# Performance work log

Measured on AMD Instinct MI355X. Metric: run time of the kernel, lower is better.

Reference implementation:

```python
import jax, jax.numpy as jnp
import numpy as np

N = 64        # n_nodes per graph
H = 128       # hidden channels (128x0e + 128x1o)
NB = 8        # radial bessel basis size
L = 2         # num_interactions
R_MAX = 5.0
AVG_NEIGH = 63.0
DIM = 3       # output vector dim
B = 64        # batch (vmapped)
T = 32        # time-embedding dim
S = 5         # num_species


def _edges(n):
    # fully-connected graph, no self loops (static shapes, jit-friendly)
    s, r = np.meshgrid(np.arange(n), np.arange(n), indexing='ij')
    m = s != r
    return jnp.asarray(s[m]), jnp.asarray(r[m])


def setup_inputs() -> dict:
    key = jax.random.key(0)
    ks = jax.random.split(key, 12)
    sc = 0.05
    return {
        'positions': jax.random.normal(ks[0], (B, N, 3), jnp.float32),
        'node_features': jax.random.randint(ks[1], (B, N), 0, S).astype(jnp.int64),
        'global_features': jax.random.normal(ks[2], (B, T), jnp.float32),
        'emb': jax.random.normal(ks[3], (S, H), jnp.float32) * sc,
        'Wt': jax.random.normal(ks[4], (T, H), jnp.float32) * sc,
        'Wr1': jax.random.normal(ks[5], (L, NB, H), jnp.float32) * sc,
        'Wr2': jax.random.normal(ks[6], (L, H, H), jnp.float32) * sc,
        'Wupd': jax.random.normal(ks[7], (L, H, H), jnp.float32) * sc,
        'Wmix': jax.random.normal(ks[8], (L, H, H), jnp.float32) * sc,
        'Wg1': jax.random.normal(ks[9], (H, H), jnp.float32) * sc,
        'Wg2': jax.random.normal(ks[10], (H, H), jnp.float32) * sc,
        'final_scaling': jnp.ones((), jnp.float32),
    }


def _call_single(pos, z, t, emb, Wt, Wr1, Wr2, Wupd, Wmix, Wg1, Wg2, final_scaling):
    snd, rcv = _edges(N)
    ev = pos[rcv] - pos[snd]                               # [E,3] edge vectors (gather)
    r = jnp.sqrt(jnp.sum(ev * ev, axis=-1) + 1e-12)        # [E]
    u = ev / r[:, None]                                    # unit directions
    # Bessel radial basis with cosine cutoff (r_max acts as soft radius graph)
    n = jnp.arange(1, NB + 1, dtype=pos.dtype)
    rb = jnp.sin(n * jnp.pi * r[:, None] / R_MAX) / r[:, None]   # [E,NB]
    fc = 0.5 * (jnp.cos(jnp.pi * r / R_MAX) + 1.0) * (r < R_MAX)
    rb = rb * fc[:, None]
    # node embedding from species + time embedding
    h = emb[z] + t @ Wt                                    # [N,H] scalar features
    v = jnp.zeros((N, H, DIM), pos.dtype)                  # vector (1o) features
    for l in range(L):
        w = jax.nn.silu(rb @ Wr1[l]) @ Wr2[l]              # [E,H] radial weights
        m0 = w * h[snd]                                    # [E,H] scalar messages
        m1 = m0[:, :, None] * u[:, None, :]                # [E,H,3] vector messages
        a0 = jax.ops.segment_sum(m0, rcv, num_segments=N) / AVG_NEIGH
        a1 = jax.ops.segment_sum(m1, rcv, num_segments=N) / AVG_NEIGH
        h = h + a0 @ Wupd[l]
        v = v + jnp.einsum('ngd,gh->nhd', a1, Wmix[l])
    # equivariant readout: scalar gate per channel contracts vector channels
    g = jax.nn.silu(h @ Wg1) @ Wg2                         # [N,H]
    out = jnp.einsum('nhd,nh->nd', v, g)                   # [N,3]
    return out * final_scaling


def reference(positions, node_features, global_features, emb, Wt, Wr1, Wr2, Wupd, Wmix, Wg1, Wg2, final_scaling):
    f = lambda p, z, t: _call_single(p, z, t, emb, Wt, Wr1, Wr2, Wupd, Wmix, Wg1, Wg2, final_scaling)
    return jax.vmap(f)(positions, node_features, global_features)
```

## Files before the change

kernel.cpp:

```cpp
#include <hip/hip_runtime.h>
#include <math.h>

#define NN 64
#define HH 128
#define NBB 8
#define TT 32
#define BB 64
#define NROW (BB * NN)
#define PLANE ((size_t)NROW * HH)
#define WR1OFF (8 * 16384)

typedef __attribute__((ext_vector_type(8))) short short8;
typedef __attribute__((ext_vector_type(4))) float f32x4;
typedef __attribute__((ext_vector_type(2))) float f32x2;
typedef __attribute__((ext_vector_type(2))) unsigned int u32x2;

__device__ __forceinline__ float silu_f(float x) {
  return x * __builtin_amdgcn_rcpf(1.0f + __expf(-x));
}

__device__ __forceinline__ unsigned short bf1(float x) {
  __bf16 h = (__bf16)x;
  return *(unsigned short*)&h;
}
__device__ __forceinline__ unsigned bf2(float lo, float hi) {
  return (unsigned)bf1(lo) | ((unsigned)bf1(hi) << 16);
}

__device__ __forceinline__ void gemm8(
    const unsigned short (*sA)[136], const unsigned short* __restrict__ Bp,
    int w, int nlo, int quad, f32x4 C[2]) {
  const short8 z8 = {0, 0, 0, 0, 0, 0, 0, 0};
  short8 afr[4];
#pragma unroll
  for (int kt = 0; kt < 4; ++kt)
    afr[kt] = (nlo < 8) ? *(const short8*)&sA[nlo][kt * 32 + quad * 8] : z8;
#pragma unroll
  for (int nt = 0; nt < 2; ++nt)
#pragma unroll
    for (int kt = 0; kt < 4; ++kt) {
      short8 bfr = *(const short8*)&Bp[((kt * 128 + w * 32 + nt * 16 + nlo) * 4 + quad) * 8];
      C[nt] = __builtin_amdgcn_mfma_f32_16x16x32_bf16(afr[kt], bfr, C[nt], 0, 0, 0);
    }
}

__global__ __launch_bounds__(256) void k_init(
    const float* __restrict__ emb, const int* __restrict__ z,
    const float* __restrict__ gf, const float* __restrict__ Wt,
    const float* __restrict__ Wr1, const float* __restrict__ Wr2,
    const float* __restrict__ Wupd, const float* __restrict__ Wmix,
    const float* __restrict__ Wg1, const float* __restrict__ Wg2,
    float* __restrict__ h, unsigned short* __restrict__ Wpack) {
  __shared__ float tvec[HH];
  __shared__ int sz[NN];
  int b4 = blockIdx.x, tid = threadIdx.x;
  {
    int p2 = b4 * 256 + tid;
    int p = p2 * 2;
    int m = p >> 14;
    int j = p & 7;
    int q = (p >> 3) & 3;
    int n = (p >> 5) & 127;
    int kt = (p >> 12) & 3;
    int k = kt * 32 + q * 8 + j;
    const float* src;
    int base;
    if (m < 2) { src = Wr2; base = m * 16384; }
    else if (m < 4) { src = Wupd; base = (m - 2) * 16384; }
    else if (m < 6) { src = Wmix; base = (m - 4) * 16384; }
    else if (m == 6) { src = Wg1; base = 0; }
    else { src = Wg2; base = 0; }
    float v0 = src[base + k * 128 + n];
    float v1 = src[base + (k + 1) * 128 + n];
    *(unsigned*)&Wpack[p] = bf2(v0, v1);
  }
  if (tid < 32) {
    int e = b4 * 32 + tid;
    int l = e >> 12, p = e & 4095;
    int n = p >> 5, q = (p >> 3) & 3, j = p & 7;
    float val = (q == 0) ? Wr1[l * NBB * HH + j * HH + n] : 0.f;
    Wpack[WR1OFF + l * 4096 + p] = bf1(val);
  }
  if (b4 < 64) {
    int b = b4;
    if (tid < NN) sz[tid] = z[b * NN + tid];
    if (tid < HH) {
      float acc = 0.f;
#pragma unroll
      for (int k = 0; k < TT; ++k) acc += gf[b * TT + k] * Wt[k * HH + tid];
      tvec[tid] = acc;
    }
    __syncthreads();
    for (int i = tid; i < NN * HH; i += 256) {
      int n = i >> 7, c = i & 127;
      h[(size_t)b * NN * HH + i] = emb[sz[n] * HH + c] + tvec[c];
    }
  }
}

__global__ __launch_bounds__(256) void k_layer(
    const float* __restrict__ pos,
    const float* __restrict__ hA,
    const unsigned short* __restrict__ a0in,
    unsigned short* __restrict__ apout,
    const unsigned short* __restrict__ Wpack,
    int l) {
  __shared__ __align__(16) unsigned short sh_S[NN][136];
  __shared__ __align__(16) unsigned short sh_M0T[4][32][72];
  __shared__ __align__(16) unsigned short sh_rbh[2][NN][8];
  __shared__ __align__(16) unsigned short sh_ub[2][4][NN];

  int blk = blockIdx.x;
  int b = blk >> 4, rp4 = blk & 15;
  int r0 = rp4 * 4;
  int tid = threadIdx.x;
  int w = tid >> 6, lane = tid & 63;
  int nlo = lane & 15, quad = lane >> 4;

  f32x4 hbv[4][2];
#pragma unroll
  for (int mt = 0; mt < 4; ++mt)
#pragma unroll
    for (int nt = 0; nt < 2; ++nt)
#pragma unroll
      for (int reg = 0; reg < 4; ++reg)
        hbv[mt][nt][reg] =
            hA[((size_t)b * NN + mt * 16 + quad * 4 + reg) * HH + w * 32 + nt * 16 + nlo];

  const unsigned short* Wr1p = Wpack + WR1OFF + l * 4096;
  short8 bw[2];
#pragma unroll
  for (int nt = 0; nt < 2; ++nt)
    bw[nt] = *(const short8*)&Wr1p[((w * 32 + nt * 16 + nlo) * 4 + quad) * 8];
  const unsigned short* Bbase = Wpack + l * 16384;
  short8 bfr[4][2];
#pragma unroll
  for (int kt = 0; kt < 4; ++kt)
#pragma unroll
    for (int nt = 0; nt < 2; ++nt)
      bfr[kt][nt] = *(const short8*)&Bbase[((kt * 128 + w * 32 + nt * 16 + nlo) * 4 + quad) * 8];

  const short8 zero8 = {0, 0, 0, 0, 0, 0, 0, 0};

#pragma unroll
  for (int pp = 0; pp < 2; ++pp) {
    int rb0 = r0 + pp * 2;

    {
      int s = tid & 63;
      int ksel = (tid >> 6) & 1;
      int ri = (tid >> 7) & 1;
      int r = rb0 + ri;
      const float* pb = pos + b * NN * 3;
      float dx = pb[r * 3 + 0] - pb[s * 3 + 0];
      float dy = pb[r * 3 + 1] - pb[s * 3 + 1];
      float dz = pb[r * 3 + 2] - pb[s * 3 + 2];
      float rr = sqrtf(dx * dx + dy * dy + dz * dz + 1e-12f);
      float inv = __builtin_amdgcn_rcpf(rr);
      const float invAvg = 1.0f / 63.0f;
      if (ksel == 0) {
        float ia = inv * invAvg;
        sh_ub[ri][1][s] = bf1(dx * ia);
        sh_ub[ri][2][s] = bf1(dy * ia);
        sh_ub[ri][3][s] = bf1(dz * ia);
      } else {
        sh_ub[ri][0][s] = bf1(invAvg);
      }
      const float PI_OVER_5 = 0.628318530717958647692f;
      float fc = (s != r && rr < 5.0f) ? 0.5f * (__cosf(PI_OVER_5 * rr) + 1.0f) : 0.0f;
      float base = PI_OVER_5 * rr;
      float sc = inv * fc;
      int k0 = ksel * 4;
      float v0 = __sinf((float)(k0 + 1) * base) * sc;
      float v1 = __sinf((float)(k0 + 2) * base) * sc;
      float v2 = __sinf((float)(k0 + 3) * base) * sc;
      float v3 = __sinf((float)(k0 + 4) * base) * sc;
      *(unsigned*)&sh_rbh[ri][s][k0]     = bf2(v0, v1);
      *(unsigned*)&sh_rbh[ri][s][k0 + 2] = bf2(v2, v3);
    }
    if (pp == 0 && l) {
      for (int i = tid; i < NN * 64; i += 256) {
        int s = i >> 6, c2 = (i & 63) * 2;
        *(unsigned*)&sh_S[s][c2] =
            *(const unsigned*)&a0in[((size_t)b * NN + s) * HH + c2];
      }
    }
    __syncthreads();

    if (pp == 0 && l) {
      const unsigned short* Bu = Wpack + 2 * 16384;
#pragma unroll
      for (int mt = 0; mt < 4; ++mt) {
        short8 afr[4];
#pragma unroll
        for (int kt = 0; kt < 4; ++kt)
          afr[kt] = *(const short8*)&sh_S[mt * 16 + nlo][kt * 32 + quad * 8];
#pragma unroll
        for (int nt = 0; nt < 2; ++nt)
#pragma unroll
          for (int kt = 0; kt < 4; ++kt) {
            short8 bfr2 = *(const short8*)&Bu[((kt * 128 + w * 32 + nt * 16 + nlo) * 4 + quad) * 8];
            hbv[mt][nt] = __builtin_amdgcn_mfma_f32_16x16x32_bf16(afr[kt], bfr2, hbv[mt][nt], 0, 0, 0);
          }
      }
      __syncthreads();
    }

    short8 au[2][2];
#pragma unroll
    for (int ri = 0; ri < 2; ++ri)
#pragma unroll
      for (int kt = 0; kt < 2; ++kt)
        au[ri][kt] = (nlo < 4) ? *(const short8*)&sh_ub[ri][nlo][kt * 32 + quad * 8] : zero8;

#pragma unroll
    for (int ri = 0; ri < 2; ++ri) {
#pragma unroll
      for (int mtp = 0; mtp < 2; ++mtp) {
        f32x4 Cs[2][2];
#pragma unroll
        for (int mi = 0; mi < 2; ++mi)
#pragma unroll
          for (int nt = 0; nt < 2; ++nt) Cs[mi][nt] = (f32x4){0.f, 0.f, 0.f, 0.f};
#pragma unroll
        for (int mi = 0; mi < 2; ++mi) {
          int mt = mtp * 2 + mi;
          short8 afr = (quad == 0) ? *(const short8*)&sh_rbh[ri][mt * 16 + nlo][0] : zero8;
#pragma unroll
          for (int nt = 0; nt < 2; ++nt)
            Cs[mi][nt] = __builtin_amdgcn_mfma_f32_16x16x32_bf16(afr, bw[nt], Cs[mi][nt], 0, 0, 0);
        }
#pragma unroll
        for (int mi = 0; mi < 2; ++mi)
#pragma unroll
          for (int nt = 0; nt < 2; ++nt)
#pragma unroll
            for (int reg = 0; reg < 4; ++reg) {
              int s = (mtp * 2 + mi) * 16 + quad * 4 + reg;
              int c = w * 32 + nt * 16 + nlo;
              sh_S[s][c] = bf1(silu_f(Cs[mi][nt][reg]));
            }
      }
      __syncthreads();

#pragma unroll
      for (int mt = 0; mt < 4; ++mt) {
        short8 afr[4];
        int s_a = mt * 16 + nlo;
#pragma unroll
        for (int kt = 0; kt < 4; ++kt)
          afr[kt] = *(const short8*)&sh_S[s_a][kt * 32 + quad * 8];
#pragma unroll
        for (int nt = 0; nt < 2; ++nt) {
          f32x4 C = {0.f, 0.f, 0.f, 0.f};
#pragma unroll
          for (int kt = 0; kt < 4; ++kt)
            C = __builtin_amdgcn_mfma_f32_16x16x32_bf16(afr[kt], bfr[kt][nt], C, 0, 0, 0);
          f32x4 m0 = C * hbv[mt][nt];
          u32x2 pk;
          pk.x = bf2(m0[0], m0[1]);
          pk.y = bf2(m0[2], m0[3]);
          *(u32x2*)&sh_M0T[w][nt * 16 + nlo][mt * 16 + quad * 4] = pk;
        }
      }
      {
        f32x4 Cu[2] = {{0, 0, 0, 0}, {0, 0, 0, 0}};
#pragma unroll
        for (int nt = 0; nt < 2; ++nt)
#pragma unroll
          for (int kt = 0; kt < 2; ++kt) {
            short8 bm = *(const short8*)&sh_M0T[w][nt * 16 + nlo][kt * 32 + quad * 8];
            Cu[nt] = __builtin_amdgcn_mfma_f32_16x16x32_bf16(au[ri][kt], bm, Cu[nt], 0, 0, 0);
          }
        if (quad == 0) {
#pragma unroll
          for (int nt = 0; nt < 2; ++nt) {
            size_t base = (size_t)(b * NN + rb0 + ri) * HH + w * 32 + nt * 16 + nlo;
#pragma unroll
            for (int reg = 0; reg < 4; ++reg)
              apout[(l * 4 + reg) * PLANE + base] = bf1(Cu[nt][reg]);
          }
        }
      }
      if (!(pp == 1 && ri == 1)) __syncthreads();
    }
  }
}

__global__ __launch_bounds__(256) void k_update_ro(
    const unsigned short* __restrict__ apbf, const float* __restrict__ hA,
    const unsigned short* __restrict__ Wpack,
    const float* __restrict__ fs, float* __restrict__ out) {
  __shared__ __align__(16) unsigned short sh_a[8][8][136];
  __shared__ __align__(16) unsigned short sh_h[8][136];
  __shared__ float red[4][8][3];
  int tid = threadIdx.x, w = tid >> 6, lane = tid & 63;
  int nlo = lane & 15, quad = lane >> 4;
  int row0 = blockIdx.x * 8;
  for (int i = tid; i < 8 * 8 * 64; i += 256) {
    int p = i >> 9, rr = (i >> 6) & 7, c2 = (i & 63) * 2;
    *(unsigned*)&sh_a[p][rr][c2] =
        *(const unsigned*)&apbf[p * PLANE + (size_t)(row0 + rr) * HH + c2];
  }
  f32x4 Ch[2];
#pragma unroll
  for (int nt = 0; nt < 2; ++nt)
#pragma unroll
    for (int reg = 0; reg < 4; ++reg)
      Ch[nt][reg] = (quad < 2)
          ? hA[(size_t)(row0 + quad * 4 + reg) * HH + w * 32 + nt * 16 + nlo] : 0.f;
  __syncthreads();
  gemm8(sh_a[0], Wpack + 2 * 16384, w, nlo, quad, Ch);
  gemm8(sh_a[4], Wpack + 3 * 16384, w, nlo, quad, Ch);
  f32x4 Cx[2] = {{0,0,0,0},{0,0,0,0}};
  f32x4 Cy[2] = {{0,0,0,0},{0,0,0,0}};
  f32x4 Cz[2] = {{0,0,0,0},{0,0,0,0}};
  gemm8(sh_a[1], Wpack + 4 * 16384, w, nlo, quad, Cx);
  gemm8(sh_a[5], Wpack + 5 * 16384, w, nlo, quad, Cx);
  gemm8(sh_a[2], Wpack + 4 * 16384, w, nlo, quad, Cy);
  gemm8(sh_a[6], Wpack + 5 * 16384, w, nlo, quad, Cy);
  gemm8(sh_a[3], Wpack + 4 * 16384, w, nlo, quad, Cz);
  gemm8(sh_a[7], Wpack + 5 * 16384, w, nlo, quad, Cz);
  if (quad < 2) {
#pragma unroll
    for (int nt = 0; nt < 2; ++nt)
#pragma unroll
      for (int reg = 0; reg < 4; ++reg)
        sh_h[quad * 4 + reg][w * 32 + nt * 16 + nlo] = bf1(Ch[nt][reg]);
  }
  __syncthreads();
  unsigned short (*sh_q)[136] = sh_a[0];
  f32x4 Cq[2] = {{0,0,0,0},{0,0,0,0}};
  gemm8(sh_h, Wpack + 6 * 16384, w, nlo, quad, Cq);
  if (quad < 2) {
#pragma unroll
    for (int nt = 0; nt < 2; ++nt)
#pragma unroll
      for (int reg = 0; reg < 4; ++reg)
        sh_q[quad * 4 + reg][w * 32 + nt * 16 + nlo] = bf1(silu_f(Cq[nt][reg]));
  }
  __syncthreads();
  f32x4 Cg[2] = {{0,0,0,0},{0,0,0,0}};
  gemm8(sh_q, Wpack + 7 * 16384, w, nlo, quad, Cg);
  float pr[3][4];
#pragma unroll
  for (int d = 0; d < 3; ++d)
#pragma unroll
    for (int reg = 0; reg < 4; ++reg) pr[d][reg] = 0.f;
#pragma unroll
  for (int nt = 0; nt < 2; ++nt)
#pragma unroll
    for (int reg = 0; reg < 4; ++reg) {
      float gv = Cg[nt][reg];
      pr[0][reg] += gv * Cx[nt][reg];
      pr[1][reg] += gv * Cy[nt][reg];
      pr[2][reg] += gv * Cz[nt][reg];
    }
#pragma unroll
  for (int off = 1; off < 16; off <<= 1)
#pragma unroll
    for (int d = 0; d < 3; ++d)
#pragma unroll
      for (int reg = 0; reg < 4; ++reg)
        pr[d][reg] += __shfl_xor(pr[d][reg], off);
  if (nlo == 0 && quad < 2) {
#pragma unroll
    for (int d = 0; d < 3; ++d)
#pragma unroll
      for (int reg = 0; reg < 4; ++reg)
        red[w][quad * 4 + reg][d] = pr[d][reg];
  }
  __syncthreads();
  if (tid < 24) {
    int row = tid / 3, d = tid % 3;
    float s = red[0][row][d] + red[1][row][d] + red[2][row][d] + red[3][row][d];
    out[(size_t)(row0 + row) * 3 + d] = s * fs[0];
  }
}

extern "C" void kernel_launch(void* const* d_in, const int* in_sizes, int n_in,
                              void* d_out, int out_size, void* d_ws, size_t ws_size,
                              hipStream_t stream) {
  const float* pos  = (const float*)d_in[0];
  const int*   z    = (const int*)d_in[1];
  const float* gf   = (const float*)d_in[2];
  const float* emb  = (const float*)d_in[3];
  const float* Wt   = (const float*)d_in[4];
  const float* Wr1  = (const float*)d_in[5];
  const float* Wr2  = (const float*)d_in[6];
  const float* Wupd = (const float*)d_in[7];
  const float* Wmix = (const float*)d_in[8];
  const float* Wg1  = (const float*)d_in[9];
  const float* Wg2  = (const float*)d_in[10];
  const float* fs   = (const float*)d_in[11];
  float* out = (float*)d_out;

  float* ws = (float*)d_ws;
  float* hA = ws;
  unsigned short* apbf = (unsigned short*)(ws + PLANE);
  unsigned short* Wpack = (unsigned short*)(ws + 5 * PLANE);

  k_init<<<dim3(256), dim3(256), 0, stream>>>(emb, z, gf, Wt, Wr1, Wr2, Wupd,
                                              Wmix, Wg1, Wg2, hA, Wpack);
  k_layer<<<dim3(BB * 16), dim3(256), 0, stream>>>(pos, hA, apbf, apbf, Wpack, 0);
  k_layer<<<dim3(BB * 16), dim3(256), 0, stream>>>(pos, hA, apbf, apbf, Wpack, 1);
  k_update_ro<<<dim3(512), dim3(256), 0, stream>>>(apbf, hA, Wpack, fs, out);
}
```

Baseline: 146.3 us.

## Replace MFMA edge-reduction with register shuffle reduction and double-buffer radial stage

The per-receiver aggregation over senders, previously done by writing bf16 messages to shared memory and running an extra MFMA against a unit-vector matrix, now happens in fp32 registers with cross-lane shuffles. Unit vectors are stored as fp32 in shared memory. The radial SiLU buffer is double-buffered so the second receiver's radial stage can run before the first receiver's main GEMM, which removes a barrier. Launch bounds now request 4 blocks per SM, which may force register spilling given the large register-resident fragments.

```diff
diff --git a/kernel.cpp b/kernel.cpp
--- a/kernel.cpp
+++ b/kernel.cpp
@@ -98,17 +98,16 @@
   }
 }
 
-__global__ __launch_bounds__(256) void k_layer(
+__global__ __launch_bounds__(256, 4) void k_layer(
     const float* __restrict__ pos,
     const float* __restrict__ hA,
     const unsigned short* __restrict__ a0in,
     unsigned short* __restrict__ apout,
     const unsigned short* __restrict__ Wpack,
     int l) {
-  __shared__ __align__(16) unsigned short sh_S[NN][136];
-  __shared__ __align__(16) unsigned short sh_M0T[4][32][72];
+  __shared__ __align__(16) unsigned short sh_S[2][NN][136];
   __shared__ __align__(16) unsigned short sh_rbh[2][NN][8];
-  __shared__ __align__(16) unsigned short sh_ub[2][4][NN];
+  __shared__ __align__(16) float sh_uf[2][NN][4];
 
   int blk = blockIdx.x;
   int b = blk >> 4, rp4 = blk & 15;
@@ -116,6 +115,7 @@
   int tid = threadIdx.x;
   int w = tid >> 6, lane = tid & 63;
   int nlo = lane & 15, quad = lane >> 4;
+  const float invAvg = 1.0f / 63.0f;
 
   f32x4 hbv[4][2];
 #pragma unroll
@@ -141,6 +141,82 @@
       bfr[kt][nt] = *(const short8*)&Bbase[((kt * 128 + w * 32 + nt * 16 + nlo) * 4 + quad) * 8];
 
   const short8 zero8 = {0, 0, 0, 0, 0, 0, 0, 0};
+
+  auto stageB = [&](int ri, int buf) {
+#pragma unroll
+    for (int mtp = 0; mtp < 2; ++mtp) {
+      f32x4 Cs[2][2];
+#pragma unroll
+      for (int mi = 0; mi < 2; ++mi)
+#pragma unroll
+        for (int nt = 0; nt < 2; ++nt) Cs[mi][nt] = (f32x4){0.f, 0.f, 0.f, 0.f};
+#pragma unroll
+      for (int mi = 0; mi < 2; ++mi) {
+        int mt = mtp * 2 + mi;
+        short8 afr = (quad == 0) ? *(const short8*)&sh_rbh[ri][mt * 16 + nlo][0] : zero8;
+#pragma unroll
+        for (int nt = 0; nt < 2; ++nt)
+          Cs[mi][nt] = __builtin_amdgcn_mfma_f32_16x16x32_bf16(afr, bw[nt], Cs[mi][nt], 0, 0, 0);
+      }
+#pragma unroll
+      for (int mi = 0; mi < 2; ++mi)
+#pragma unroll
+        for (int nt = 0; nt < 2; ++nt)
+#pragma unroll
+          for (int reg = 0; reg < 4; ++reg) {
+            int s = (mtp * 2 + mi) * 16 + quad * 4 + reg;
+            int c = w * 32 + nt * 16 + nlo;
+            sh_S[buf][s][c] = bf1(silu_f(Cs[mi][nt][reg]));
+          }
+    }
+  };
+
+  auto mainG = [&](int ri, int buf, int rglob) {
+    float a0[2] = {0.f, 0.f};
+    float a1[2][3] = {{0.f, 0.f, 0.f}, {0.f, 0.f, 0.f}};
+#pragma unroll
+    for (int mt = 0; mt < 4; ++mt) {
+      short8 afr[4];
+      int s_a = mt * 16 + nlo;
+#pragma unroll
+      for (int kt = 0; kt < 4; ++kt)
+        afr[kt] = *(const short8*)&sh_S[buf][s_a][kt * 32 + quad * 8];
+      f32x4 u3[4];
+#pragma unroll
+      for (int reg = 0; reg < 4; ++reg)
+        u3[reg] = *(const f32x4*)&sh_uf[ri][mt * 16 + quad * 4 + reg][0];
+#pragma unroll
+      for (int nt = 0; nt < 2; ++nt) {
+        f32x4 C = {0.f, 0.f, 0.f, 0.f};
+#pragma unroll
+        for (int kt = 0; kt < 4; ++kt)
+          C = __builtin_amdgcn_mfma_f32_16x16x32_bf16(afr[kt], bfr[kt][nt], C, 0, 0, 0);
+#pragma unroll
+        for (int reg = 0; reg < 4; ++reg) {
+          float m0 = C[reg] * hbv[mt][nt][reg];
+          a0[nt] += m0;
+          a1[nt][0] += u3[reg][0] * m0;
+          a1[nt][1] += u3[reg][1] * m0;
+          a1[nt][2] += u3[reg][2] * m0;
+        }
+      }
+    }
+#pragma unroll
+    for (int nt = 0; nt < 2; ++nt) {
+      float v0 = a0[nt], v1 = a1[nt][0], v2 = a1[nt][1], v3 = a1[nt][2];
+      v0 += __shfl_xor(v0, 16); v0 += __shfl_xor(v0, 32);
+      v1 += __shfl_xor(v1, 16); v1 += __shfl_xor(v1, 32);
+      v2 += __shfl_xor(v2, 16); v2 += __shfl_xor(v2, 32);
+      v3 += __shfl_xor(v3, 16); v3 += __shfl_xor(v3, 32);
+      if (quad == 0) {
+        size_t base = (size_t)(b * NN + rglob) * HH + w * 32 + nt * 16 + nlo;
+        apout[(l * 4 + 0) * PLANE + base] = bf1(v0 * invAvg);
+        apout[(l * 4 + 1) * PLANE + base] = bf1(v1);
+        apout[(l * 4 + 2) * PLANE + base] = bf1(v2);
+        apout[(l * 4 + 3) * PLANE + base] = bf1(v3);
+      }
+    }
+  };
 
 #pragma unroll
   for (int pp = 0; pp < 2; ++pp) {
@@ -157,14 +233,11 @@
       float dz = pb[r * 3 + 2] - pb[s * 3 + 2];
       float rr = sqrtf(dx * dx + dy * dy + dz * dz + 1e-12f);
       float inv = __builtin_amdgcn_rcpf(rr);
-      const float invAvg = 1.0f / 63.0f;
       if (ksel == 0) {
         float ia = inv * invAvg;
-        sh_ub[ri][1][s] = bf1(dx * ia);
-        sh_ub[ri][2][s] = bf1(dy * ia);
-        sh_ub[ri][3][s] = bf1(dz * ia);
-      } else {
-        sh_ub[ri][0][s] = bf1(invAvg);
+        sh_uf[ri][s][0] = dx * ia;
+        sh_uf[ri][s][1] = dy * ia;
+        sh_uf[ri][s][2] = dz * ia;
       }
       const float PI_OVER_5 = 0.628318530717958647692f;
       float fc = (s != r && rr < 5.0f) ? 0.5f * (__cosf(PI_OVER_5 * rr) + 1.0f) : 0.0f;
@@ -181,7 +254,7 @@
     if (pp == 0 && l) {
       for (int i = tid; i < NN * 64; i += 256) {
         int s = i >> 6, c2 = (i & 63) * 2;
-        *(unsigned*)&sh_S[s][c2] =
+        *(unsigned*)&sh_S[0][s][c2] =
             *(const unsigned*)&a0in[((size_t)b * NN + s) * HH + c2];
       }
     }
@@ -194,7 +267,7 @@
         short8 afr[4];
 #pragma unroll
         for (int kt = 0; kt < 4; ++kt)
-          afr[kt] = *(const short8*)&sh_S[mt * 16 + nlo][kt * 32 + quad * 8];
+          afr[kt] = *(const short8*)&sh_S[0][mt * 16 + nlo][kt * 32 + quad * 8];
 #pragma unroll
         for (int nt = 0; nt < 2; ++nt)
 #pragma unroll
@@ -206,84 +279,13 @@
       __syncthreads();
     }
 
-    short8 au[2][2];
-#pragma unroll
-    for (int ri = 0; ri < 2; ++ri)
-#pragma unroll
-      for (int kt = 0; kt < 2; ++kt)
-        au[ri][kt] = (nlo < 4) ? *(const short8*)&sh_ub[ri][nlo][kt * 32 + quad * 8] : zero8;
-
-#pragma unroll
-    for (int ri = 0; ri < 2; ++ri) {
-#pragma unroll
-      for (int mtp = 0; mtp < 2; ++mtp) {
-        f32x4 Cs[2][2];
-#pragma unroll
-        for (int mi = 0; mi < 2; ++mi)
-#pragma unroll
-          for (int nt = 0; nt < 2; ++nt) Cs[mi][nt] = (f32x4){0.f, 0.f, 0.f, 0.f};
-#pragma unroll
-        for (int mi = 0; mi < 2; ++mi) {
-          int mt = mtp * 2 + mi;
-          short8 afr = (quad == 0) ? *(const short8*)&sh_rbh[ri][mt * 16 + nlo][0] : zero8;
-#pragma unroll
-          for (int nt = 0; nt < 2; ++nt)
-            Cs[mi][nt] = __builtin_amdgcn_mfma_f32_16x16x32_bf16(afr, bw[nt], Cs[mi][nt], 0, 0, 0);
-        }
-#pragma unroll
-        for (int mi = 0; mi < 2; ++mi)
-#pragma unroll
-          for (int nt = 0; nt < 2; ++nt)
-#pragma unroll
-            for (int reg = 0; reg < 4; ++reg) {
-              int s = (mtp * 2 + mi) * 16 + quad * 4 + reg;
-              int c = w * 32 + nt * 16 + nlo;
-              sh_S[s][c] = bf1(silu_f(Cs[mi][nt][reg]));
-            }
-      }
-      __syncthreads();
-
-#pragma unroll
-      for (int mt = 0; mt < 4; ++mt) {
-        short8 afr[4];
-        int s_a = mt * 16 + nlo;
-#pragma unroll
-        for (int kt = 0; kt < 4; ++kt)
-          afr[kt] = *(const short8*)&sh_S[s_a][kt * 32 + quad * 8];
-#pragma unroll
-        for (int nt = 0; nt < 2; ++nt) {
-          f32x4 C = {0.f, 0.f, 0.f, 0.f};
-#pragma unroll
-          for (int kt = 0; kt < 4; ++kt)
-            C = __builtin_amdgcn_mfma_f32_16x16x32_bf16(afr[kt], bfr[kt][nt], C, 0, 0, 0);
-          f32x4 m0 = C * hbv[mt][nt];
-          u32x2 pk;
-          pk.x = bf2(m0[0], m0[1]);
-          pk.y = bf2(m0[2], m0[3]);
-          *(u32x2*)&sh_M0T[w][nt * 16 + nlo][mt * 16 + quad * 4] = pk;
-        }
-      }
-      {
-        f32x4 Cu[2] = {{0, 0, 0, 0}, {0, 0, 0, 0}};
-#pragma unroll
-        for (int nt = 0; nt < 2; ++nt)
-#pragma unroll
-          for (int kt = 0; kt < 2; ++kt) {
-            short8 bm = *(const short8*)&sh_M0T[w][nt * 16 + nlo][kt * 32 + quad * 8];
-            Cu[nt] = __builtin_amdgcn_mfma_f32_16x16x32_bf16(au[ri][kt], bm, Cu[nt], 0, 0, 0);
-          }
-        if (quad == 0) {
-#pragma unroll
-          for (int nt = 0; nt < 2; ++nt) {
-            size_t base = (size_t)(b * NN + rb0 + ri) * HH + w * 32 + nt * 16 + nlo;
-#pragma unroll
-            for (int reg = 0; reg < 4; ++reg)
-              apout[(l * 4 + reg) * PLANE + base] = bf1(Cu[nt][reg]);
-          }
-        }
-      }
-      if (!(pp == 1 && ri == 1)) __syncthreads();
-    }
+    stageB(0, 0);
+    __syncthreads();
+    stageB(1, 1);
+    mainG(0, 0, rb0 + 0);
+    __syncthreads();
+    mainG(1, 1, rb0 + 1);
+    if (pp == 0) __syncthreads();
   }
 }
 
```

After: 222.6 us. 52.1% more time.

## Swizzle LDS tiles, vectorize update staging loads, spread init embedding work

Applied to the files above, without the earlier changes.

Applies an XOR swizzle to column indices of the shared-memory A-operand tiles (sh_S, sh_a, sh_h, sh_q), so MFMA fragment reads and scalar scatter writes spread across LDS banks. Replaces the 4-byte staging loop in the update/readout kernel with 16-byte vector loads and stores. Spreads the node-embedding initialization across all init blocks, 16 nodes each, instead of only the first 64 blocks. The swizzle has to be applied consistently at every read and write site; a missed site would silently corrupt results.

```diff
diff --git a/kernel.cpp b/kernel.cpp
--- a/kernel.cpp
+++ b/kernel.cpp
@@ -10,7 +10,10 @@
 #define PLANE ((size_t)NROW * HH)
 #define WR1OFF (8 * 16384)
 
+#define SWZ(s, c) ((c) ^ (((s) & 7) << 4))
+
 typedef __attribute__((ext_vector_type(8))) short short8;
+typedef __attribute__((ext_vector_type(8))) unsigned short ushort8;
 typedef __attribute__((ext_vector_type(4))) float f32x4;
 typedef __attribute__((ext_vector_type(2))) float f32x2;
 typedef __attribute__((ext_vector_type(2))) unsigned int u32x2;
@@ -34,7 +37,7 @@
   short8 afr[4];
 #pragma unroll
   for (int kt = 0; kt < 4; ++kt)
-    afr[kt] = (nlo < 8) ? *(const short8*)&sA[nlo][kt * 32 + quad * 8] : z8;
+    afr[kt] = (nlo < 8) ? *(const short8*)&sA[nlo][SWZ(nlo, kt * 32 + quad * 8)] : z8;
 #pragma unroll
   for (int nt = 0; nt < 2; ++nt)
 #pragma unroll
@@ -52,7 +55,7 @@
     const float* __restrict__ Wg1, const float* __restrict__ Wg2,
     float* __restrict__ h, unsigned short* __restrict__ Wpack) {
   __shared__ float tvec[HH];
-  __shared__ int sz[NN];
+  __shared__ int sz[16];
   int b4 = blockIdx.x, tid = threadIdx.x;
   {
     int p2 = b4 * 256 + tid;
@@ -81,9 +84,10 @@
     float val = (q == 0) ? Wr1[l * NBB * HH + j * HH + n] : 0.f;
     Wpack[WR1OFF + l * 4096 + p] = bf1(val);
   }
-  if (b4 < 64) {
-    int b = b4;
-    if (tid < NN) sz[tid] = z[b * NN + tid];
+  {
+    int b = b4 >> 2;
+    int n0 = (b4 & 3) * 16;
+    if (tid < 16) sz[tid] = z[b * NN + n0 + tid];
     if (tid < HH) {
       float acc = 0.f;
 #pragma unroll
@@ -91,9 +95,9 @@
       tvec[tid] = acc;
     }
     __syncthreads();
-    for (int i = tid; i < NN * HH; i += 256) {
+    for (int i = tid; i < 16 * HH; i += 256) {
       int n = i >> 7, c = i & 127;
-      h[(size_t)b * NN * HH + i] = emb[sz[n] * HH + c] + tvec[c];
+      h[(size_t)b * NN * HH + (n0 + n) * HH + c] = emb[sz[n] * HH + c] + tvec[c];
     }
   }
 }
@@ -181,7 +185,7 @@
     if (pp == 0 && l) {
       for (int i = tid; i < NN * 64; i += 256) {
         int s = i >> 6, c2 = (i & 63) * 2;
-        *(unsigned*)&sh_S[s][c2] =
+        *(unsigned*)&sh_S[s][SWZ(s, c2)] =
             *(const unsigned*)&a0in[((size_t)b * NN + s) * HH + c2];
       }
     }
@@ -192,9 +196,10 @@
 #pragma unroll
       for (int mt = 0; mt < 4; ++mt) {
         short8 afr[4];
+        int s_a = mt * 16 + nlo;
 #pragma unroll
         for (int kt = 0; kt < 4; ++kt)
-          afr[kt] = *(const short8*)&sh_S[mt * 16 + nlo][kt * 32 + quad * 8];
+          afr[kt] = *(const short8*)&sh_S[s_a][SWZ(s_a, kt * 32 + quad * 8)];
 #pragma unroll
         for (int nt = 0; nt < 2; ++nt)
 #pragma unroll
@@ -238,7 +243,7 @@
             for (int reg = 0; reg < 4; ++reg) {
               int s = (mtp * 2 + mi) * 16 + quad * 4 + reg;
               int c = w * 32 + nt * 16 + nlo;
-              sh_S[s][c] = bf1(silu_f(Cs[mi][nt][reg]));
+              sh_S[s][SWZ(s, c)] = bf1(silu_f(Cs[mi][nt][reg]));
             }
       }
       __syncthreads();
@@ -249,7 +254,7 @@
         int s_a = mt * 16 + nlo;
 #pragma unroll
         for (int kt = 0; kt < 4; ++kt)
-          afr[kt] = *(const short8*)&sh_S[s_a][kt * 32 + quad * 8];
+          afr[kt] = *(const short8*)&sh_S[s_a][SWZ(s_a, kt * 32 + quad * 8)];
 #pragma unroll
         for (int nt = 0; nt < 2; ++nt) {
           f32x4 C = {0.f, 0.f, 0.f, 0.f};
@@ -297,10 +302,12 @@
   int tid = threadIdx.x, w = tid >> 6, lane = tid & 63;
   int nlo = lane & 15, quad = lane >> 4;
   int row0 = blockIdx.x * 8;
-  for (int i = tid; i < 8 * 8 * 64; i += 256) {
-    int p = i >> 9, rr = (i >> 6) & 7, c2 = (i & 63) * 2;
-    *(unsigned*)&sh_a[p][rr][c2] =
-        *(const unsigned*)&apbf[p * PLANE + (size_t)(row0 + rr) * HH + c2];
+#pragma unroll
+  for (int it = 0; it < 4; ++it) {
+    int i2 = it * 256 + tid;
+    int p = i2 >> 7, rr = (i2 >> 4) & 7, c8 = (i2 & 15) * 8;
+    *(ushort8*)&sh_a[p][rr][SWZ(rr, c8)] =
+        *(const ushort8*)&apbf[p * PLANE + (size_t)(row0 + rr) * HH + c8];
   }
   f32x4 Ch[2];
 #pragma unroll
@@ -325,8 +332,10 @@
 #pragma unroll
     for (int nt = 0; nt < 2; ++nt)
 #pragma unroll
-      for (int reg = 0; reg < 4; ++reg)
-        sh_h[quad * 4 + reg][w * 32 + nt * 16 + nlo] = bf1(Ch[nt][reg]);
+      for (int reg = 0; reg < 4; ++reg) {
+        int row = quad * 4 + reg, c = w * 32 + nt * 16 + nlo;
+        sh_h[row][SWZ(row, c)] = bf1(Ch[nt][reg]);
+      }
   }
   __syncthreads();
   unsigned short (*sh_q)[136] = sh_a[0];
@@ -336,8 +345,10 @@
 #pragma unroll
     for (int nt = 0; nt < 2; ++nt)
 #pragma unroll
-      for (int reg = 0; reg < 4; ++reg)
-        sh_q[quad * 4 + reg][w * 32 + nt * 16 + nlo] = bf1(silu_f(Cq[nt][reg]));
+      for (int reg = 0; reg < 4; ++reg) {
+        int row = quad * 4 + reg, c = w * 32 + nt * 16 + nlo;
+        sh_q[row][SWZ(row, c)] = bf1(silu_f(Cq[nt][reg]));
+      }
   }
   __syncthreads();
   f32x4 Cg[2] = {{0,0,0,0},{0,0,0,0}};
```

After: 151.5 us. +3.6%, slower.

## Fuse second interaction layer with update and readout into one kernel

Applied to the files above, without the earlier changes.

Splits the generic layer kernel into a layer-0 kernel and a fused kernel. The fused kernel runs layer 1 for 8 receiver rows per block, then runs the update and readout stage for those same 8 rows, which that block just wrote. This removes one kernel launch and its inter-kernel barrier. It also halves the redundant per-block recomputation of the layer-1 node update (a0·Wupd over all 64 nodes), since 8 blocks per graph do it instead of 16. In exchange, layer 1 runs on half as many blocks, each doing twice the serial work.

```diff
diff --git a/kernel.cpp b/kernel.cpp
--- a/kernel.cpp
+++ b/kernel.cpp
@@ -12,7 +12,6 @@
 
 typedef __attribute__((ext_vector_type(8))) short short8;
 typedef __attribute__((ext_vector_type(4))) float f32x4;
-typedef __attribute__((ext_vector_type(2))) float f32x2;
 typedef __attribute__((ext_vector_type(2))) unsigned int u32x2;
 
 __device__ __forceinline__ float silu_f(float x) {
@@ -98,13 +97,9 @@
   }
 }
 
-__global__ __launch_bounds__(256) void k_layer(
-    const float* __restrict__ pos,
-    const float* __restrict__ hA,
-    const unsigned short* __restrict__ a0in,
-    unsigned short* __restrict__ apout,
-    const unsigned short* __restrict__ Wpack,
-    int l) {
+__global__ __launch_bounds__(256) void k_layer0(
+    const float* __restrict__ pos, const float* __restrict__ hA,
+    unsigned short* __restrict__ apout, const unsigned short* __restrict__ Wpack) {
   __shared__ __align__(16) unsigned short sh_S[NN][136];
   __shared__ __align__(16) unsigned short sh_M0T[4][32][72];
   __shared__ __align__(16) unsigned short sh_rbh[2][NN][8];
@@ -127,12 +122,12 @@
         hbv[mt][nt][reg] =
             hA[((size_t)b * NN + mt * 16 + quad * 4 + reg) * HH + w * 32 + nt * 16 + nlo];
 
-  const unsigned short* Wr1p = Wpack + WR1OFF + l * 4096;
+  const unsigned short* Wr1p = Wpack + WR1OFF;
   short8 bw[2];
 #pragma unroll
   for (int nt = 0; nt < 2; ++nt)
     bw[nt] = *(const short8*)&Wr1p[((w * 32 + nt * 16 + nlo) * 4 + quad) * 8];
-  const unsigned short* Bbase = Wpack + l * 16384;
+  const unsigned short* Bbase = Wpack;
   short8 bfr[4][2];
 #pragma unroll
   for (int kt = 0; kt < 4; ++kt)
@@ -145,7 +140,6 @@
 #pragma unroll
   for (int pp = 0; pp < 2; ++pp) {
     int rb0 = r0 + pp * 2;
-
     {
       int s = tid & 63;
       int ksel = (tid >> 6) & 1;
@@ -178,33 +172,7 @@
       *(unsigned*)&sh_rbh[ri][s][k0]     = bf2(v0, v1);
       *(unsigned*)&sh_rbh[ri][s][k0 + 2] = bf2(v2, v3);
     }
-    if (pp == 0 && l) {
-      for (int i = tid; i < NN * 64; i += 256) {
-        int s = i >> 6, c2 = (i & 63) * 2;
-        *(unsigned*)&sh_S[s][c2] =
-            *(const unsigned*)&a0in[((size_t)b * NN + s) * HH + c2];
-      }
-    }
     __syncthreads();
-
-    if (pp == 0 && l) {
-      const unsigned short* Bu = Wpack + 2 * 16384;
-#pragma unroll
-      for (int mt = 0; mt < 4; ++mt) {
-        short8 afr[4];
-#pragma unroll
-        for (int kt = 0; kt < 4; ++kt)
-          afr[kt] = *(const short8*)&sh_S[mt * 16 + nlo][kt * 32 + quad * 8];
-#pragma unroll
-        for (int nt = 0; nt < 2; ++nt)
-#pragma unroll
-          for (int kt = 0; kt < 4; ++kt) {
-            short8 bfr2 = *(const short8*)&Bu[((kt * 128 + w * 32 + nt * 16 + nlo) * 4 + quad) * 8];
-            hbv[mt][nt] = __builtin_amdgcn_mfma_f32_16x16x32_bf16(afr[kt], bfr2, hbv[mt][nt], 0, 0, 0);
-          }
-      }
-      __syncthreads();
-    }
 
     short8 au[2][2];
 #pragma unroll
@@ -278,7 +246,7 @@
             size_t base = (size_t)(b * NN + rb0 + ri) * HH + w * 32 + nt * 16 + nlo;
 #pragma unroll
             for (int reg = 0; reg < 4; ++reg)
-              apout[(l * 4 + reg) * PLANE + base] = bf1(Cu[nt][reg]);
+              apout[reg * PLANE + base] = bf1(Cu[nt][reg]);
           }
         }
       }
@@ -287,94 +255,275 @@
   }
 }
 
-__global__ __launch_bounds__(256) void k_update_ro(
-    const unsigned short* __restrict__ apbf, const float* __restrict__ hA,
-    const unsigned short* __restrict__ Wpack,
+__global__ __launch_bounds__(256) void k_fused(
+    const float* __restrict__ pos, const float* __restrict__ hA,
+    unsigned short* __restrict__ apbf, const unsigned short* __restrict__ Wpack,
     const float* __restrict__ fs, float* __restrict__ out) {
-  __shared__ __align__(16) unsigned short sh_a[8][8][136];
-  __shared__ __align__(16) unsigned short sh_h[8][136];
-  __shared__ float red[4][8][3];
-  int tid = threadIdx.x, w = tid >> 6, lane = tid & 63;
+  __shared__ __align__(16) unsigned char smem[38912];
+  unsigned short (*sh_S)[136]      = (unsigned short (*)[136])smem;
+  unsigned short (*sh_M0T)[32][72] = (unsigned short (*)[32][72])(smem + 17408);
+  unsigned short (*sh_rbh)[NN][8]  = (unsigned short (*)[NN][8])(smem + 35840);
+  unsigned short (*sh_ub)[4][NN]   = (unsigned short (*)[4][NN])(smem + 37888);
+
+  int blk = blockIdx.x;
+  int b = blk >> 3, u8 = blk & 7;
+  int tid = threadIdx.x;
+  int w = tid >> 6, lane = tid & 63;
   int nlo = lane & 15, quad = lane >> 4;
-  int row0 = blockIdx.x * 8;
-  for (int i = tid; i < 8 * 8 * 64; i += 256) {
-    int p = i >> 9, rr = (i >> 6) & 7, c2 = (i & 63) * 2;
-    *(unsigned*)&sh_a[p][rr][c2] =
-        *(const unsigned*)&apbf[p * PLANE + (size_t)(row0 + rr) * HH + c2];
-  }
-  f32x4 Ch[2];
+  const short8 zero8 = {0, 0, 0, 0, 0, 0, 0, 0};
+
+  f32x4 hbv[4][2];
+#pragma unroll
+  for (int mt = 0; mt < 4; ++mt)
+#pragma unroll
+    for (int nt = 0; nt < 2; ++nt)
+#pragma unroll
+      for (int reg = 0; reg < 4; ++reg)
+        hbv[mt][nt][reg] =
+            hA[((size_t)b * NN + mt * 16 + quad * 4 + reg) * HH + w * 32 + nt * 16 + nlo];
+
+  for (int i = tid; i < NN * 64; i += 256) {
+    int s = i >> 6, c2 = (i & 63) * 2;
+    *(unsigned*)&sh_S[s][c2] =
+        *(const unsigned*)&apbf[((size_t)b * NN + s) * HH + c2];
+  }
+  __syncthreads();
+  {
+    const unsigned short* Bu = Wpack + 2 * 16384;
+#pragma unroll
+    for (int mt = 0; mt < 4; ++mt) {
+      short8 afr[4];
+#pragma unroll
+      for (int kt = 0; kt < 4; ++kt)
+        afr[kt] = *(const short8*)&sh_S[mt * 16 + nlo][kt * 32 + quad * 8];
+#pragma unroll
+      for (int nt = 0; nt < 2; ++nt)
+#pragma unroll
+        for (int kt = 0; kt < 4; ++kt) {
+          short8 bfr2 = *(const short8*)&Bu[((kt * 128 + w * 32 + nt * 16 + nlo) * 4 + quad) * 8];
+          hbv[mt][nt] = __builtin_amdgcn_mfma_f32_16x16x32_bf16(afr[kt], bfr2, hbv[mt][nt], 0, 0, 0);
+        }
+    }
+  }
+  __syncthreads();
+
+  const unsigned short* Wr1p = Wpack + WR1OFF + 4096;
+  short8 bw[2];
 #pragma unroll
   for (int nt = 0; nt < 2; ++nt)
-#pragma unroll
-    for (int reg = 0; reg < 4; ++reg)
-      Ch[nt][reg] = (quad < 2)
-          ? hA[(size_t)(row0 + quad * 4 + reg) * HH + w * 32 + nt * 16 + nlo] : 0.f;
-  __syncthreads();
-  gemm8(sh_a[0], Wpack + 2 * 16384, w, nlo, quad, Ch);
-  gemm8(sh_a[4], Wpack + 3 * 16384, w, nlo, quad, Ch);
-  f32x4 Cx[2] = {{0,0,0,0},{0,0,0,0}};
-  f32x4 Cy[2] = {{0,0,0,0},{0,0,0,0}};
-  f32x4 Cz[2] = {{0,0,0,0},{0,0,0,0}};
-  gemm8(sh_a[1], Wpack + 4 * 16384, w, nlo, quad, Cx);
-  gemm8(sh_a[5], Wpack + 5 * 16384, w, nlo, quad, Cx);
-  gemm8(sh_a[2], Wpack + 4 * 16384, w, nlo, quad, Cy);
-  gemm8(sh_a[6], Wpack + 5 * 16384, w, nlo, quad, Cy);
-  gemm8(sh_a[3], Wpack + 4 * 16384, w, nlo, quad, Cz);
-  gemm8(sh_a[7], Wpack + 5 * 16384, w, nlo, quad, Cz);
-  if (quad < 2) {
+    bw[nt] = *(const short8*)&Wr1p[((w * 32 + nt * 16 + nlo) * 4 + quad) * 8];
+  const unsigned short* Bbase = Wpack + 16384;
+  short8 bfr[4][2];
+#pragma unroll
+  for (int kt = 0; kt < 4; ++kt)
 #pragma unroll
     for (int nt = 0; nt < 2; ++nt)
+      bfr[kt][nt] = *(const short8*)&Bbase[((kt * 128 + w * 32 + nt * 16 + nlo) * 4 + quad) * 8];
+
+  for (int unit = 0; unit < 2; ++unit) {
+    int r0 = (u8 * 2 + unit) * 4;
+#pragma unroll
+    for (int pp = 0; pp < 2; ++pp) {
+      int rb0 = r0 + pp * 2;
+      {
+        int s = tid & 63;
+        int ksel = (tid >> 6) & 1;
+        int ri = (tid >> 7) & 1;
+        int r = rb0 + ri;
+        const float* pb = pos + b * NN * 3;
+        float dx = pb[r * 3 + 0] - pb[s * 3 + 0];
+        float dy = pb[r * 3 + 1] - pb[s * 3 + 1];
+        float dz = pb[r * 3 + 2] - pb[s * 3 + 2];
+        float rr = sqrtf(dx * dx + dy * dy + dz * dz + 1e-12f);
+        float inv = __builtin_amdgcn_rcpf(rr);
+        const float invAvg = 1.0f / 63.0f;
+        if (ksel == 0) {
+          float ia = inv * invAvg;
+          sh_ub[ri][1][s] = bf1(dx * ia);
+          sh_ub[ri][2][s] = bf1(dy * ia);
+          sh_ub[ri][3][s] = bf1(dz * ia);
+        } else {
+          sh_ub[ri][0][s] = bf1(invAvg);
+        }
+        const float PI_OVER_5 = 0.628318530717958647692f;
+        float fc = (s != r && rr < 5.0f) ? 0.5f * (__cosf(PI_OVER_5 * rr) + 1.0f) : 0.0f;
+        float base = PI_OVER_5 * rr;
+        float sc = inv * fc;
+        int k0 = ksel * 4;
+        float v0 = __sinf((float)(k0 + 1) * base) * sc;
+        float v1 = __sinf((float)(k0 + 2) * base) * sc;
+        float v2 = __sinf((float)(k0 + 3) * base) * sc;
+        float v3 = __sinf((float)(k0 + 4) * base) * sc;
+        *(unsigned*)&sh_rbh[ri][s][k0]     = bf2(v0, v1);
+        *(unsigned*)&sh_rbh[ri][s][k0 + 2] = bf2(v2, v3);
+      }
+      __syncthreads();
+
+      short8 au[2][2];
+#pragma unroll
+      for (int ri = 0; ri < 2; ++ri)
+#pragma unroll
+        for (int kt = 0; kt < 2; ++kt)
+          au[ri][kt] = (nlo < 4) ? *(const short8*)&sh_ub[ri][nlo][kt * 32 + quad * 8] : zero8;
+
+#pragma unroll
+      for (int ri = 0; ri < 2; ++ri) {
+#pragma unroll
+        for (int mtp = 0; mtp < 2; ++mtp) {
+          f32x4 Cs[2][2];
+#pragma unroll
+          for (int mi = 0; mi < 2; ++mi)
+#pragma unroll
+            for (int nt = 0; nt < 2; ++nt) Cs[mi][nt] = (f32x4){0.f, 0.f, 0.f, 0.f};
+#pragma unroll
+          for (int mi = 0; mi < 2; ++mi) {
+            int mt = mtp * 2 + mi;
+            short8 afr = (quad == 0) ? *(const short8*)&sh_rbh[ri][mt * 16 + nlo][0] : zero8;
+#pragma unroll
+            for (int nt = 0; nt < 2; ++nt)
+              Cs[mi][nt] = __builtin_amdgcn_mfma_f32_16x16x32_bf16(afr, bw[nt], Cs[mi][nt], 0, 0, 0);
+          }
+#pragma unroll
+          for (int mi = 0; mi < 2; ++mi)
+#pragma unroll
+            for (int nt = 0; nt < 2; ++nt)
+#pragma unroll
+              for (int reg = 0; reg < 4; ++reg) {
+                int s = (mtp * 2 + mi) * 16 + quad * 4 + reg;
+                int c = w * 32 + nt * 16 + nlo;
+                sh_S[s][c] = bf1(silu_f(Cs[mi][nt][reg]));
+              }
+        }
+        __syncthreads();
+
+#pragma unroll
+        for (int mt = 0; mt < 4; ++mt) {
+          short8 afr[4];
+          int s_a = mt * 16 + nlo;
+#pragma unroll
+          for (int kt = 0; kt < 4; ++kt)
+            afr[kt] = *(const short8*)&sh_S[s_a][kt * 32 + quad * 8];
+#pragma unroll
+          for (int nt = 0; nt < 2; ++nt) {
+            f32x4 C = {0.f, 0.f, 0.f, 0.f};
+#pragma unroll
+            for (int kt = 0; kt < 4; ++kt)
+              C = __builtin_amdgcn_mfma_f32_16x16x32_bf16(afr[kt], bfr[kt][nt], C, 0, 0, 0);
+            f32x4 m0 = C * hbv[mt][nt];
+            u32x2 pk;
+            pk.x = bf2(m0[0], m0[1]);
+            pk.y = bf2(m0[2], m0[3]);
+            *(u32x2*)&sh_M0T[w][nt * 16 + nlo][mt * 16 + quad * 4] = pk;
+          }
+        }
+        {
+          f32x4 Cu[2] = {{0, 0, 0, 0}, {0, 0, 0, 0}};
+#pragma unroll
+          for (int nt = 0; nt < 2; ++nt)
+#pragma unroll
+            for (int kt = 0; kt < 2; ++kt) {
+              short8 bm = *(const short8*)&sh_M0T[w][nt * 16 + nlo][kt * 32 + quad * 8];
+              Cu[nt] = __builtin_amdgcn_mfma_f32_16x16x32_bf16(au[ri][kt], bm, Cu[nt], 0, 0, 0);
+            }
+          if (quad == 0) {
+#pragma unroll
+            for (int nt = 0; nt < 2; ++nt) {
+              size_t base = (size_t)(b * NN + rb0 + ri) * HH + w * 32 + nt * 16 + nlo;
+#pragma unroll
+              for (int reg = 0; reg < 4; ++reg)
+                apbf[(4 + reg) * PLANE + base] = bf1(Cu[nt][reg]);
+            }
+          }
+        }
+        __syncthreads();
+      }
+    }
+  }
+
+  {
+    unsigned short (*sh_a)[8][136] = (unsigned short (*)[8][136])smem;
+    unsigned short (*sh_h)[136]    = (unsigned short (*)[136])(smem + 17408);
+    float (*red)[8][3]             = (float (*)[8][3])(smem + 17408 + 2176);
+    int row0 = blk * 8;
+    for (int i = tid; i < 8 * 8 * 64; i += 256) {
+      int p = i >> 9, rr = (i >> 6) & 7, c2 = (i & 63) * 2;
+      *(unsigned*)&sh_a[p][rr][c2] =
+          *(const unsigned*)&apbf[p * PLANE + (size_t)(row0 + rr) * HH + c2];
+    }
+    f32x4 Ch[2];
+#pragma unroll
+    for (int nt = 0; nt < 2; ++nt)
 #pragma unroll
       for (int reg = 0; reg < 4; ++reg)
-        sh_h[quad * 4 + reg][w * 32 + nt * 16 + nlo] = bf1(Ch[nt][reg]);
-  }
-  __syncthreads();
-  unsigned short (*sh_q)[136] = sh_a[0];
-  f32x4 Cq[2] = {{0,0,0,0},{0,0,0,0}};
-  gemm8(sh_h, Wpack + 6 * 16384, w, nlo, quad, Cq);
-  if (quad < 2) {
+        Ch[nt][reg] = (quad < 2)
+            ? hA[(size_t)(row0 + quad * 4 + reg) * HH + w * 32 + nt * 16 + nlo] : 0.f;
+    __syncthreads();
+    gemm8(sh_a[0], Wpack + 2 * 16384, w, nlo, quad, Ch);
+    gemm8(sh_a[4], Wpack + 3 * 16384, w, nlo, quad, Ch);
+    f32x4 Cx[2] = {{0,0,0,0},{0,0,0,0}};
+    f32x4 Cy[2] = {{0,0,0,0},{0,0,0,0}};
+    f32x4 Cz[2] = {{0,0,0,0},{0,0,0,0}};
+    gemm8(sh_a[1], Wpack + 4 * 16384, w, nlo, quad, Cx);
+    gemm8(sh_a[5], Wpack + 5 * 16384, w, nlo, quad, Cx);
+    gemm8(sh_a[2], Wpack + 4 * 16384, w, nlo, quad, Cy);
+    gemm8(sh_a[6], Wpack + 5 * 16384, w, nlo, quad, Cy);
+    gemm8(sh_a[3], Wpack + 4 * 16384, w, nlo, quad, Cz);
+    gemm8(sh_a[7], Wpack + 5 * 16384, w, nlo, quad, Cz);
+    if (quad < 2) {
+#pragma unroll
+      for (int nt = 0; nt < 2; ++nt)
+#pragma unroll
+        for (int reg = 0; reg < 4; ++reg)
+          sh_h[quad * 4 + reg][w * 32 + nt * 16 + nlo] = bf1(Ch[nt][reg]);
+    }
+    __syncthreads();
+    unsigned short (*sh_q)[136] = sh_a[0];
+    f32x4 Cq[2] = {{0,0,0,0},{0,0,0,0}};
+    gemm8(sh_h, Wpack + 6 * 16384, w, nlo, quad, Cq);
+    if (quad < 2) {
+#pragma unroll
+      for (int nt = 0; nt < 2; ++nt)
+#pragma unroll
+        for (int reg = 0; reg < 4; ++reg)
+          sh_q[quad * 4 + reg][w * 32 + nt * 16 + nlo] = bf1(silu_f(Cq[nt][reg]));
+    }
+    __syncthreads();
+    f32x4 Cg[2] = {{0,0,0,0},{0,0,0,0}};
+    gemm8(sh_q, Wpack + 7 * 16384, w, nlo, quad, Cg);
+    float pr[3][4];
+#pragma unroll
+    for (int d = 0; d < 3; ++d)
+#pragma unroll
+      for (int reg = 0; reg < 4; ++reg) pr[d][reg] = 0.f;
 #pragma unroll
     for (int nt = 0; nt < 2; ++nt)
 #pragma unroll
-      for (int reg = 0; reg < 4; ++reg)
-        sh_q[quad * 4 + reg][w * 32 + nt * 16 + nlo] = bf1(silu_f(Cq[nt][reg]));
-  }
-  __syncthreads();
-  f32x4 Cg[2] = {{0,0,0,0},{0,0,0,0}};
-  gemm8(sh_q, Wpack + 7 * 16384, w, nlo, quad, Cg);
-  float pr[3][4];
-#pragma unroll
-  for (int d = 0; d < 3; ++d)
-#pragma unroll
-    for (int reg = 0; reg < 4; ++reg) pr[d][reg] = 0.f;
-#pragma unroll
-  for (int nt = 0; nt < 2; ++nt)
-#pragma unroll
-    for (int reg = 0; reg < 4; ++reg) {
-      float gv = Cg[nt][reg];
-      pr[0][reg] += gv * Cx[nt][reg];
-      pr[1][reg] += gv * Cy[nt][reg];
-      pr[2][reg] += gv * Cz[nt][reg];
-    }
-#pragma unroll
-  for (int off = 1; off < 16; off <<= 1)
-#pragma unroll
-    for (int d = 0; d < 3; ++d)
-#pragma unroll
-      for (int reg = 0; reg < 4; ++reg)
-        pr[d][reg] += __shfl_xor(pr[d][reg], off);
-  if (nlo == 0 && quad < 2) {
-#pragma unroll
-    for (int d = 0; d < 3; ++d)
-#pragma unroll
-      for (int reg = 0; reg < 4; ++reg)
-        red[w][quad * 4 + reg][d] = pr[d][reg];
-  }
-  __syncthreads();
-  if (tid < 24) {
-    int row = tid / 3, d = tid % 3;
-    float s = red[0][row][d] + red[1][row][d] + red[2][row][d] + red[3][row][d];
-    out[(size_t)(row0 + row) * 3 + d] = s * fs[0];
+      for (int reg = 0; reg < 4; ++reg) {
+        float gv = Cg[nt][reg];
+        pr[0][reg] += gv * Cx[nt][reg];
+        pr[1][reg] += gv * Cy[nt][reg];
+        pr[2][reg] += gv * Cz[nt][reg];
+      }
+#pragma unroll
+    for (int off = 1; off < 16; off <<= 1)
+#pragma unroll
+      for (int d = 0; d < 3; ++d)
+#pragma unroll
+        for (int reg = 0; reg < 4; ++reg)
+          pr[d][reg] += __shfl_xor(pr[d][reg], off);
+    if (nlo == 0 && quad < 2) {
+#pragma unroll
+      for (int d = 0; d < 3; ++d)
+#pragma unroll
+        for (int reg = 0; reg < 4; ++reg)
+          red[w][quad * 4 + reg][d] = pr[d][reg];
+    }
+    __syncthreads();
+    if (tid < 24) {
+      int row = tid / 3, d = tid % 3;
+      float s = red[0][row][d] + red[1][row][d] + red[2][row][d] + red[3][row][d];
+      out[(size_t)(row0 + row) * 3 + d] = s * fs[0];
+    }
   }
 }
 
@@ -402,7 +551,6 @@
 
   k_init<<<dim3(256), dim3(256), 0, stream>>>(emb, z, gf, Wt, Wr1, Wr2, Wupd,
                                               Wmix, Wg1, Wg2, hA, Wpack);
-  k_layer<<<dim3(BB * 16), dim3(256), 0, stream>>>(pos, hA, apbf, apbf, Wpack, 0);
-  k_layer<<<dim3(BB * 16), dim3(256), 0, stream>>>(pos, hA, apbf, apbf, Wpack, 1);
-  k_update_ro<<<dim3(512), dim3(256), 0, stream>>>(apbf, hA, Wpack, fs, out);
-}
+  k_layer0<<<dim3(BB * 16), dim3(256), 0, stream>>>(pos, hA, apbf, Wpack);
+  k_fused<<<dim3(512), dim3(256), 0, stream>>>(pos, hA, apbf, Wpack, fs, out);
+}
```

Result: faster. 141.3 us (-3.4%).
